# Performance work log

Measured on AMD Instinct MI355X. Metric: run time of the kernel, lower is better.

The kernel has to match this reference:

```python
import jax, jax.numpy as jnp
import numpy as np

B, T, C = 4, 1024, 1024
H, D = 16, 64


def setup_inputs() -> dict:
    key = jax.random.key(0)
    ks = jax.random.split(key, 5)
    sc = 0.02
    x = jax.random.normal(ks[0], (B, T, C), dtype=jnp.float32)
    Wq = jax.random.normal(ks[1], (H, C, D), dtype=jnp.float32) * sc
    Wk = jax.random.normal(ks[2], (H, C, D), dtype=jnp.float32) * sc
    Wv = jax.random.normal(ks[3], (H, C, D), dtype=jnp.float32) * sc
    Wp = jax.random.normal(ks[4], (H * D, C), dtype=jnp.float32) * sc
    bp = jnp.zeros((C,), dtype=jnp.float32)
    return {"x": x, "Wq": Wq, "Wk": Wk, "Wv": Wv, "Wp": Wp, "bp": bp}


def reference(x, Wq, Wk, Wv, Wp, bp):
    # per-head projections (bias-free, as in nanoGPT Head)
    q = jnp.einsum('btc,hcd->bhtd', x, Wq)
    k = jnp.einsum('btc,hcd->bhtd', x, Wk)
    v = jnp.einsum('btc,hcd->bhtd', x, Wv)
    scale = 1.0 / jnp.sqrt(jnp.asarray(D, dtype=x.dtype))
    scores = jnp.einsum('bhtd,bhsd->bhts', q, k) * scale  # [B,H,T,T]
    causal = jnp.tril(jnp.ones((T, T), dtype=bool))
    scores = jnp.where(causal, scores, jnp.asarray(-jnp.inf, dtype=scores.dtype))
    attn = jax.nn.softmax(scores, axis=-1)
    out = jnp.einsum('bhts,bhsd->bhtd', attn, v)  # [B,H,T,D]
    out = out.transpose(0, 2, 1, 3).reshape(B, T, H * D)  # concat heads
    return out @ Wp + bp  # final projection (dropout=0)
```

## Files before the change

kernel.cpp:

```cpp
#include <hip/hip_runtime.h>
#include <hip/hip_bf16.h>

typedef unsigned short u16;
typedef __bf16 bf16x8 __attribute__((ext_vector_type(8)));
typedef float floatx4 __attribute__((ext_vector_type(4)));

#define SB 4
#define ST 1024
#define SC 1024
#define SH 16
#define SD 64

__device__ __forceinline__ u16 f2bf(float f) {
    unsigned int u = __builtin_bit_cast(unsigned int, f);
    u += 0x7fffu + ((u >> 16) & 1u);
    return (u16)(u >> 16);
}

__device__ __forceinline__ void gload16(const u16* g, u16* l) {
    __builtin_amdgcn_global_load_lds(
        (const __attribute__((address_space(1))) unsigned int*)g,
        (__attribute__((address_space(3))) unsigned int*)l, 16, 0, 0);
}

__global__ void k_prep(const float* __restrict__ x,
                       const float* __restrict__ Wq, const float* __restrict__ Wk,
                       const float* __restrict__ Wv, const float* __restrict__ Wp,
                       u16* __restrict__ xb, u16* __restrict__ Wqkv, u16* __restrict__ Wpt) {
    __shared__ float tile[64 * 65];
    const int id = blockIdx.x, tid = threadIdx.x;
    if (id < 4096) {
        int i = id * 256 + tid;
        float4 v = ((const float4*)x)[i];
        uint2 o;
        o.x = (unsigned)f2bf(v.x) | ((unsigned)f2bf(v.y) << 16);
        o.y = (unsigned)f2bf(v.z) | ((unsigned)f2bf(v.w) << 16);
        ((uint2*)xb)[i] = o;
    } else if (id < 4864) {
        const int id1 = id - 4096;
        const int qkv = id1 >> 8, rem = id1 & 255, h = rem >> 4, c0 = (rem & 15) * 64;
        const float* src = qkv == 0 ? Wq : (qkv == 1 ? Wk : Wv);
        #pragma unroll
        for (int i = 0; i < 16; ++i) {
            int idx = tid + i * 256;
            int r = idx >> 6, d = idx & 63;
            tile[r * 65 + d] = src[(h * SC + c0 + r) * SD + d];
        }
        __syncthreads();
        #pragma unroll
        for (int i = 0; i < 16; ++i) {
            int idx = tid + i * 256;
            int d = idx >> 6, cc = idx & 63;
            Wqkv[(qkv * 1024 + h * SD + d) * SC + c0 + cc] = f2bf(tile[cc * 65 + d]);
        }
    } else {
        const int id2 = id - 4864;
        const int n0 = (id2 & 15) * 64, k0 = (id2 >> 4) * 64;
        #pragma unroll
        for (int i = 0; i < 16; ++i) {
            int idx = tid + i * 256;
            int r = idx >> 6, nn = idx & 63;
            tile[r * 65 + nn] = Wp[(k0 + r) * SC + n0 + nn];
        }
        __syncthreads();
        #pragma unroll
        for (int i = 0; i < 16; ++i) {
            int idx = tid + i * 256;
            int nr = idx >> 6, kk = idx & 63;
            Wpt[(n0 + nr) * (SH * SD) + k0 + kk] = f2bf(tile[kk * 65 + nr]);
        }
    }
}

__launch_bounds__(256)
__global__ void k_gemm(const u16* __restrict__ A, const u16* __restrict__ Bt,
                       int M, int N, int K,
                       u16* __restrict__ Qb, u16* __restrict__ Kb, u16* __restrict__ Vt) {
    constexpr int BM = 128, BN = 64, SM = 4, SN = 2;
    __shared__ u16 Als[2][BM * 64];
    __shared__ u16 Bls[2][BN * 64];
    const int tid = threadIdx.x, lane = tid & 63, w = tid >> 6;
    const int quad = lane >> 4, l16 = lane & 15;
    const int sr = lane >> 3, sc = lane & 7;
    const int nt = N / BN;
    const int m0 = (blockIdx.x / nt) * BM, n0 = (blockIdx.x % nt) * BN;
    const int wm = (w >> 1) * 64, wn = (w & 1) * 32;

    auto stage = [&](int buf, int k0) {
        #pragma unroll
        for (int i = 0; i < 4; ++i) {
            int rb = (w * 4 + i) * 8;
            gload16(&A[(long)(m0 + rb + sr) * K + k0 + ((sc ^ sr) << 3)], &Als[buf][rb * 64]);
        }
        #pragma unroll
        for (int i = 0; i < 2; ++i) {
            int rb = (w * 2 + i) * 8;
            gload16(&Bt[(long)(n0 + rb + sr) * K + k0 + ((sc ^ sr) << 3)], &Bls[buf][rb * 64]);
        }
    };

    floatx4 acc[SM][SN] = {};
    const int niter = K / 64;
    stage(0, 0);
    for (int it = 0; it < niter; ++it) {
        const int buf = it & 1;
        __syncthreads();
        if (it + 1 < niter) stage(buf ^ 1, (it + 1) * 64);
        bf16x8 af[SM][2], bfr[SN][2];
        #pragma unroll
        for (int sm = 0; sm < SM; ++sm) {
            int row = wm + sm * 16 + l16;
            #pragma unroll
            for (int ks = 0; ks < 2; ++ks)
                af[sm][ks] = *(const bf16x8*)&Als[buf][row * 64 + (((ks * 4 + quad) ^ (row & 7)) << 3)];
        }
        #pragma unroll
        for (int sn = 0; sn < SN; ++sn) {
            int row = wn + sn * 16 + l16;
            #pragma unroll
            for (int ks = 0; ks < 2; ++ks)
                bfr[sn][ks] = *(const bf16x8*)&Bls[buf][row * 64 + (((ks * 4 + quad) ^ (row & 7)) << 3)];
        }
        #pragma unroll
        for (int ks = 0; ks < 2; ++ks)
            #pragma unroll
            for (int sm = 0; sm < SM; ++sm)
                #pragma unroll
                for (int sn = 0; sn < SN; ++sn)
                    acc[sm][sn] = __builtin_amdgcn_mfma_f32_16x16x32_bf16(bfr[sn][ks], af[sm][ks], acc[sm][sn], 0, 0, 0);
    }
    const int qkv = n0 >> 10, h = (n0 & 1023) >> 6;
    const float qs = qkv == 0 ? 0.18033688011112042f : 1.0f;
    #pragma unroll
    for (int sm = 0; sm < SM; ++sm) {
        const int m = m0 + wm + sm * 16 + l16;
        const int bb = m >> 10, t = m & 1023;
        #pragma unroll
        for (int sn = 0; sn < SN; ++sn) {
            const int d0 = wn + sn * 16 + (quad << 2);
            u16 pk[4];
            #pragma unroll
            for (int r = 0; r < 4; ++r) pk[r] = f2bf(acc[sm][sn][r] * qs);
            if (qkv == 2) {
                const long vb = (long)(bb * SH + h) * SD * ST + t;
                #pragma unroll
                for (int r = 0; r < 4; ++r) Vt[vb + (long)(d0 + r) * ST] = pk[r];
            } else {
                u16* dst = qkv == 0 ? Qb : Kb;
                *(uint2*)&dst[(((long)(bb * SH + h) * ST + t) << 6) + d0] = *(uint2*)pk;
            }
        }
    }
}

__launch_bounds__(256)
__global__ void k_oproj(const u16* __restrict__ A, const u16* __restrict__ Bt,
                        const float* __restrict__ bias, float* __restrict__ Cout) {
    constexpr int K = 1024, N = 1024;
    __shared__ u16 Als[4][64 * 64];
    __shared__ u16 Bls[4][64 * 64];
    const int tid = threadIdx.x, lane = tid & 63, w = tid >> 6;
    const int quad = lane >> 4, l16 = lane & 15;
    const int sr = lane >> 3, sc = lane & 7;
    const int m0 = (blockIdx.x >> 4) * 64, n0 = (blockIdx.x & 15) * 64;
    const int wm = (w >> 1) * 32, wn = (w & 1) * 32;

    floatx4 acc[2][2] = {};
    for (int kb = 0; kb < 4; ++kb) {
        const int k0 = kb * 256;
        #pragma unroll
        for (int seg = 0; seg < 4; ++seg) {
            #pragma unroll
            for (int i = 0; i < 2; ++i) {
                int rb = (w * 2 + i) * 8;
                gload16(&A[(long)(m0 + rb + sr) * K + k0 + seg * 64 + ((sc ^ sr) << 3)], &Als[seg][rb * 64]);
                gload16(&Bt[(long)(n0 + rb + sr) * K + k0 + seg * 64 + ((sc ^ sr) << 3)], &Bls[seg][rb * 64]);
            }
        }
        __syncthreads();
        #pragma unroll
        for (int seg = 0; seg < 4; ++seg) {
            bf16x8 af[2][2], bfr[2][2];
            #pragma unroll
            for (int sm = 0; sm < 2; ++sm) {
                int row = wm + sm * 16 + l16;
                #pragma unroll
                for (int ks = 0; ks < 2; ++ks)
                    af[sm][ks] = *(const bf16x8*)&Als[seg][row * 64 + (((ks * 4 + quad) ^ (row & 7)) << 3)];
            }
            #pragma unroll
            for (int sn = 0; sn < 2; ++sn) {
                int row = wn + sn * 16 + l16;
                #pragma unroll
                for (int ks = 0; ks < 2; ++ks)
                    bfr[sn][ks] = *(const bf16x8*)&Bls[seg][row * 64 + (((ks * 4 + quad) ^ (row & 7)) << 3)];
            }
            #pragma unroll
            for (int ks = 0; ks < 2; ++ks)
                #pragma unroll
                for (int sm = 0; sm < 2; ++sm)
                    #pragma unroll
                    for (int sn = 0; sn < 2; ++sn)
                        acc[sm][sn] = __builtin_amdgcn_mfma_f32_16x16x32_bf16(bfr[sn][ks], af[sm][ks], acc[sm][sn], 0, 0, 0);
        }
        if (kb < 3) __syncthreads();
    }
    #pragma unroll
    for (int sn = 0; sn < 2; ++sn) {
        const int nb = n0 + wn + sn * 16 + (quad << 2);
        const float4 bv = *(const float4*)&bias[nb];
        #pragma unroll
        for (int sm = 0; sm < 2; ++sm) {
            const int m = m0 + wm + sm * 16 + l16;
            float4 o;
            o.x = acc[sm][sn][0] + bv.x;
            o.y = acc[sm][sn][1] + bv.y;
            o.z = acc[sm][sn][2] + bv.z;
            o.w = acc[sm][sn][3] + bv.w;
            *(float4*)&Cout[(long)m * N + nb] = o;
        }
    }
}

__launch_bounds__(256)
__global__ void k_attn(const u16* __restrict__ Qg, const u16* __restrict__ Kg,
                       const u16* __restrict__ Vtg, u16* __restrict__ Og) {
    __shared__ u16 Kls[2][64 * 64];
    __shared__ u16 Vls[2][64 * 64];
    __shared__ u16 Pls[64 * 64];
    const int tid = threadIdx.x, lane = tid & 63, w = tid >> 6;
    const int quad = lane >> 4, l16 = lane & 15;
    const int sr = lane >> 3, sc = lane & 7;
    const int tile = 15 - (blockIdx.x >> 6);
    const int bh = blockIdx.x & 63;
    const int t0 = tile * 64;
    const int b = bh >> 4, h = bh & 15;
    const u16* Qbh = Qg + (long)bh * ST * SD;
    const u16* Kbh = Kg + (long)bh * ST * SD;
    const u16* Vbh = Vtg + (long)bh * SD * ST;

    bf16x8 qf[2];
    {
        const u16* qrow = Qbh + (t0 + w * 16 + l16) * SD;
        qf[0] = *(const bf16x8*)&qrow[quad * 8];
        qf[1] = *(const bf16x8*)&qrow[32 + quad * 8];
    }
    floatx4 oacc[4] = {};
    float lsum = 0.f;
    const int myt = t0 + w * 16 + l16;
    const int rowP = w * 16 + l16;

    auto stage = [&](int buf, int s0) {
        #pragma unroll
        for (int i = 0; i < 2; ++i) {
            int rb = (w * 2 + i) * 8;
            gload16(&Kbh[(s0 + rb + sr) * SD + ((sc ^ sr) << 3)], &Kls[buf][rb * 64]);
            gload16(&Vbh[(rb + sr) * ST + s0 + ((sc ^ sr) << 3)], &Vls[buf][rb * 64]);
        }
    };

    stage(0, 0);
    for (int j = 0; j <= tile; ++j) {
        const int buf = j & 1;
        const int s0 = j * 64;
        __syncthreads();
        if (j < tile) stage(buf ^ 1, s0 + 64);

        floatx4 sa[4] = {};
        #pragma unroll
        for (int sn = 0; sn < 4; ++sn) {
            int row = sn * 16 + l16;
            #pragma unroll
            for (int ks = 0; ks < 2; ++ks) {
                bf16x8 kf = *(const bf16x8*)&Kls[buf][row * 64 + (((ks * 4 + quad) ^ (row & 7)) << 3)];
                sa[sn] = __builtin_amdgcn_mfma_f32_16x16x32_bf16(kf, qf[ks], sa[sn], 0, 0, 0);
            }
        }
        const bool diag = (j == tile);
        #pragma unroll
        for (int sn = 0; sn < 4; ++sn) {
            const int sl = sn * 16 + (quad << 2);
            u16 pk[4];
            #pragma unroll
            for (int r = 0; r < 4; ++r) {
                float e = __builtin_exp2f(sa[sn][r]);
                if (diag && s0 + sl + r > myt) e = 0.f;
                lsum += e;
                pk[r] = (u16)(__builtin_bit_cast(unsigned int, e) >> 16);
            }
            *(uint2*)&Pls[rowP * 64 + (((sl >> 3) ^ (rowP & 7)) << 3) + ((quad & 1) << 2)] = *(uint2*)pk;
        }
        bf16x8 pf[2];
        #pragma unroll
        for (int ks = 0; ks < 2; ++ks)
            pf[ks] = *(const bf16x8*)&Pls[rowP * 64 + (((ks * 4 + quad) ^ (rowP & 7)) << 3)];
        #pragma unroll
        for (int dn = 0; dn < 4; ++dn) {
            int row = dn * 16 + l16;
            #pragma unroll
            for (int ks = 0; ks < 2; ++ks) {
                bf16x8 vf = *(const bf16x8*)&Vls[buf][row * 64 + (((ks * 4 + quad) ^ (row & 7)) << 3)];
                oacc[dn] = __builtin_amdgcn_mfma_f32_16x16x32_bf16(vf, pf[ks], oacc[dn], 0, 0, 0);
            }
        }
    }
    float l = lsum;
    l += __shfl_xor(l, 16);
    l += __shfl_xor(l, 32);
    const float inv = 1.0f / l;
    const long obase = ((long)(b * ST + myt) << 10) + h * SD;
    #pragma unroll
    for (int dn = 0; dn < 4; ++dn) {
        u16 pk[4];
        #pragma unroll
        for (int r = 0; r < 4; ++r) pk[r] = f2bf(oacc[dn][r] * inv);
        *(uint2*)&Og[obase + dn * 16 + (quad << 2)] = *(uint2*)pk;
    }
}

extern "C" void kernel_launch(void* const* d_in, const int* in_sizes, int n_in,
                              void* d_out, int out_size, void* d_ws, size_t ws_size,
                              hipStream_t stream) {
    const float* x  = (const float*)d_in[0];
    const float* Wq = (const float*)d_in[1];
    const float* Wk = (const float*)d_in[2];
    const float* Wv = (const float*)d_in[3];
    const float* Wp = (const float*)d_in[4];
    const float* bp = (const float*)d_in[5];
    float* out = (float*)d_out;

    char* ws = (char*)d_ws;
    u16* xb   = (u16*)(ws);
    u16* Wqkv = (u16*)(ws + (8ll  << 20));
    u16* Wpt  = (u16*)(ws + (14ll << 20));
    u16* Qb   = (u16*)(ws + (16ll << 20));
    u16* Kb   = (u16*)(ws + (24ll << 20));
    u16* Vt   = (u16*)(ws + (32ll << 20));
    u16* Ob   = (u16*)(ws + (40ll << 20));

    k_prep<<<5120, 256, 0, stream>>>(x, Wq, Wk, Wv, Wp, xb, Wqkv, Wpt);
    k_gemm<<<32 * 48, 256, 0, stream>>>(xb, Wqkv, 4096, 3072, 1024, Qb, Kb, Vt);
    k_attn<<<1024, 256, 0, stream>>>(Qb, Kb, Vt, Ob);
    k_oproj<<<1024, 256, 0, stream>>>(Ob, Wpt, bp, out);
}
```

Baseline: 161.1 us.

## Process 128 query rows per attention block to reuse K/V tiles

The attention kernel now handles a 128-row query tile per block, with each wave owning two 16-row subtiles. Every K/V tile staged in LDS therefore feeds twice as many MFMAs, halving global K/V traffic and the grid size to 512 blocks. The trade-off is more registers per thread (doubled accumulators and score tiles), a larger P buffer in LDS, coarser causal work imbalance, and fewer blocks to fill the CUs. The last two key tiles are masked on the diagonal.

```diff
diff --git a/kernel.cpp b/kernel.cpp
--- a/kernel.cpp
+++ b/kernel.cpp
@@ -227,28 +227,30 @@
                        const u16* __restrict__ Vtg, u16* __restrict__ Og) {
     __shared__ u16 Kls[2][64 * 64];
     __shared__ u16 Vls[2][64 * 64];
-    __shared__ u16 Pls[64 * 64];
+    __shared__ u16 Pls[128 * 64];
     const int tid = threadIdx.x, lane = tid & 63, w = tid >> 6;
     const int quad = lane >> 4, l16 = lane & 15;
     const int sr = lane >> 3, sc = lane & 7;
-    const int tile = 15 - (blockIdx.x >> 6);
+    const int qt = 7 - (blockIdx.x >> 6);
     const int bh = blockIdx.x & 63;
-    const int t0 = tile * 64;
+    const int t0 = qt * 128;
     const int b = bh >> 4, h = bh & 15;
     const u16* Qbh = Qg + (long)bh * ST * SD;
     const u16* Kbh = Kg + (long)bh * ST * SD;
     const u16* Vbh = Vtg + (long)bh * SD * ST;
 
-    bf16x8 qf[2];
-    {
-        const u16* qrow = Qbh + (t0 + w * 16 + l16) * SD;
-        qf[0] = *(const bf16x8*)&qrow[quad * 8];
-        qf[1] = *(const bf16x8*)&qrow[32 + quad * 8];
-    }
-    floatx4 oacc[4] = {};
-    float lsum = 0.f;
-    const int myt = t0 + w * 16 + l16;
-    const int rowP = w * 16 + l16;
+    bf16x8 qf[2][2];
+    int myt[2], rowP[2];
+    #pragma unroll
+    for (int mi = 0; mi < 2; ++mi) {
+        rowP[mi] = w * 32 + mi * 16 + l16;
+        myt[mi] = t0 + rowP[mi];
+        const u16* qrow = Qbh + (long)myt[mi] * SD;
+        qf[mi][0] = *(const bf16x8*)&qrow[quad * 8];
+        qf[mi][1] = *(const bf16x8*)&qrow[32 + quad * 8];
+    }
+    floatx4 oacc[2][4] = {};
+    float lsum[2] = {};
 
     auto stage = [&](int buf, int s0) {
         #pragma unroll
@@ -259,62 +261,73 @@
         }
     };
 
+    const int jn = 2 * qt + 2;
     stage(0, 0);
-    for (int j = 0; j <= tile; ++j) {
+    for (int j = 0; j < jn; ++j) {
         const int buf = j & 1;
         const int s0 = j * 64;
         __syncthreads();
-        if (j < tile) stage(buf ^ 1, s0 + 64);
-
-        floatx4 sa[4] = {};
+        if (j + 1 < jn) stage(buf ^ 1, s0 + 64);
+
+        floatx4 sa[2][4] = {};
         #pragma unroll
         for (int sn = 0; sn < 4; ++sn) {
             int row = sn * 16 + l16;
             #pragma unroll
             for (int ks = 0; ks < 2; ++ks) {
                 bf16x8 kf = *(const bf16x8*)&Kls[buf][row * 64 + (((ks * 4 + quad) ^ (row & 7)) << 3)];
-                sa[sn] = __builtin_amdgcn_mfma_f32_16x16x32_bf16(kf, qf[ks], sa[sn], 0, 0, 0);
-            }
-        }
-        const bool diag = (j == tile);
-        #pragma unroll
-        for (int sn = 0; sn < 4; ++sn) {
-            const int sl = sn * 16 + (quad << 2);
-            u16 pk[4];
-            #pragma unroll
-            for (int r = 0; r < 4; ++r) {
-                float e = __builtin_exp2f(sa[sn][r]);
-                if (diag && s0 + sl + r > myt) e = 0.f;
-                lsum += e;
-                pk[r] = (u16)(__builtin_bit_cast(unsigned int, e) >> 16);
-            }
-            *(uint2*)&Pls[rowP * 64 + (((sl >> 3) ^ (rowP & 7)) << 3) + ((quad & 1) << 2)] = *(uint2*)pk;
-        }
-        bf16x8 pf[2];
-        #pragma unroll
-        for (int ks = 0; ks < 2; ++ks)
-            pf[ks] = *(const bf16x8*)&Pls[rowP * 64 + (((ks * 4 + quad) ^ (rowP & 7)) << 3)];
+                sa[0][sn] = __builtin_amdgcn_mfma_f32_16x16x32_bf16(kf, qf[0][ks], sa[0][sn], 0, 0, 0);
+                sa[1][sn] = __builtin_amdgcn_mfma_f32_16x16x32_bf16(kf, qf[1][ks], sa[1][sn], 0, 0, 0);
+            }
+        }
+        const bool diag = (j >= jn - 2);
+        #pragma unroll
+        for (int mi = 0; mi < 2; ++mi) {
+            #pragma unroll
+            for (int sn = 0; sn < 4; ++sn) {
+                const int sl = sn * 16 + (quad << 2);
+                u16 pk[4];
+                #pragma unroll
+                for (int r = 0; r < 4; ++r) {
+                    float e = __builtin_exp2f(sa[mi][sn][r]);
+                    if (diag && s0 + sl + r > myt[mi]) e = 0.f;
+                    lsum[mi] += e;
+                    pk[r] = (u16)(__builtin_bit_cast(unsigned int, e) >> 16);
+                }
+                *(uint2*)&Pls[rowP[mi] * 64 + (((sl >> 3) ^ (rowP[mi] & 7)) << 3) + ((quad & 1) << 2)] = *(uint2*)pk;
+            }
+        }
+        bf16x8 pf[2][2];
+        #pragma unroll
+        for (int mi = 0; mi < 2; ++mi)
+            #pragma unroll
+            for (int ks = 0; ks < 2; ++ks)
+                pf[mi][ks] = *(const bf16x8*)&Pls[rowP[mi] * 64 + (((ks * 4 + quad) ^ (rowP[mi] & 7)) << 3)];
         #pragma unroll
         for (int dn = 0; dn < 4; ++dn) {
             int row = dn * 16 + l16;
             #pragma unroll
             for (int ks = 0; ks < 2; ++ks) {
                 bf16x8 vf = *(const bf16x8*)&Vls[buf][row * 64 + (((ks * 4 + quad) ^ (row & 7)) << 3)];
-                oacc[dn] = __builtin_amdgcn_mfma_f32_16x16x32_bf16(vf, pf[ks], oacc[dn], 0, 0, 0);
-            }
-        }
-    }
-    float l = lsum;
-    l += __shfl_xor(l, 16);
-    l += __shfl_xor(l, 32);
-    const float inv = 1.0f / l;
-    const long obase = ((long)(b * ST + myt) << 10) + h * SD;
+                oacc[0][dn] = __builtin_amdgcn_mfma_f32_16x16x32_bf16(vf, pf[0][ks], oacc[0][dn], 0, 0, 0);
+                oacc[1][dn] = __builtin_amdgcn_mfma_f32_16x16x32_bf16(vf, pf[1][ks], oacc[1][dn], 0, 0, 0);
+            }
+        }
+    }
     #pragma unroll
-    for (int dn = 0; dn < 4; ++dn) {
-        u16 pk[4];
-        #pragma unroll
-        for (int r = 0; r < 4; ++r) pk[r] = f2bf(oacc[dn][r] * inv);
-        *(uint2*)&Og[obase + dn * 16 + (quad << 2)] = *(uint2*)pk;
+    for (int mi = 0; mi < 2; ++mi) {
+        float l = lsum[mi];
+        l += __shfl_xor(l, 16);
+        l += __shfl_xor(l, 32);
+        const float inv = 1.0f / l;
+        const long obase = ((long)(b * ST + myt[mi]) << 10) + h * SD;
+        #pragma unroll
+        for (int dn = 0; dn < 4; ++dn) {
+            u16 pk[4];
+            #pragma unroll
+            for (int r = 0; r < 4; ++r) pk[r] = f2bf(oacc[mi][dn][r] * inv);
+            *(uint2*)&Og[obase + dn * 16 + (quad << 2)] = *(uint2*)pk;
+        }
     }
 }
 
@@ -340,6 +353,6 @@
 
     k_prep<<<5120, 256, 0, stream>>>(x, Wq, Wk, Wv, Wp, xb, Wqkv, Wpt);
     k_gemm<<<32 * 48, 256, 0, stream>>>(xb, Wqkv, 4096, 3072, 1024, Qb, Kb, Vt);
-    k_attn<<<1024, 256, 0, stream>>>(Qb, Kb, Vt, Ob);
+    k_attn<<<512, 256, 0, stream>>>(Qb, Kb, Vt, Ob);
     k_oproj<<<1024, 256, 0, stream>>>(Ob, Wpt, bp, out);
 }
```

New measurement: 171.8 us. 6.7% more time.

## Shrink QKV GEMM K-tile to 32 and double-buffer output projection

Applied to the files above, without the earlier changes.

The QKV projection GEMM now stages 32-wide K slices instead of 64, which halves its LDS footprint and doubles the number of loop iterations and barriers. Its swizzle is changed to a 4-way XOR to match. The output projection drops its load-all-then-compute scheme over 256-wide chunks in favour of a 64-wide double-buffered pipeline that overlaps global-to-LDS loads with MFMA. This cuts LDS use so more blocks can be resident, at the cost of more synchronisation per unit of work.

```diff
diff --git a/kernel.cpp b/kernel.cpp
--- a/kernel.cpp
+++ b/kernel.cpp
@@ -77,57 +77,50 @@
                        int M, int N, int K,
                        u16* __restrict__ Qb, u16* __restrict__ Kb, u16* __restrict__ Vt) {
     constexpr int BM = 128, BN = 64, SM = 4, SN = 2;
-    __shared__ u16 Als[2][BM * 64];
-    __shared__ u16 Bls[2][BN * 64];
+    __shared__ u16 Als[2][BM * 32];
+    __shared__ u16 Bls[2][BN * 32];
     const int tid = threadIdx.x, lane = tid & 63, w = tid >> 6;
     const int quad = lane >> 4, l16 = lane & 15;
-    const int sr = lane >> 3, sc = lane & 7;
+    const int sr = lane >> 2, sc = lane & 3;
     const int nt = N / BN;
     const int m0 = (blockIdx.x / nt) * BM, n0 = (blockIdx.x % nt) * BN;
     const int wm = (w >> 1) * 64, wn = (w & 1) * 32;
 
     auto stage = [&](int buf, int k0) {
         #pragma unroll
-        for (int i = 0; i < 4; ++i) {
-            int rb = (w * 4 + i) * 8;
-            gload16(&A[(long)(m0 + rb + sr) * K + k0 + ((sc ^ sr) << 3)], &Als[buf][rb * 64]);
-        }
-        #pragma unroll
         for (int i = 0; i < 2; ++i) {
-            int rb = (w * 2 + i) * 8;
-            gload16(&Bt[(long)(n0 + rb + sr) * K + k0 + ((sc ^ sr) << 3)], &Bls[buf][rb * 64]);
+            int rb = (w * 2 + i) * 16;
+            gload16(&A[(long)(m0 + rb + sr) * K + k0 + ((sc ^ (sr & 3)) << 3)], &Als[buf][rb * 32]);
+        }
+        {
+            int rb = w * 16;
+            gload16(&Bt[(long)(n0 + rb + sr) * K + k0 + ((sc ^ (sr & 3)) << 3)], &Bls[buf][rb * 32]);
         }
     };
 
     floatx4 acc[SM][SN] = {};
-    const int niter = K / 64;
+    const int niter = K / 32;
     stage(0, 0);
     for (int it = 0; it < niter; ++it) {
         const int buf = it & 1;
         __syncthreads();
-        if (it + 1 < niter) stage(buf ^ 1, (it + 1) * 64);
-        bf16x8 af[SM][2], bfr[SN][2];
+        if (it + 1 < niter) stage(buf ^ 1, (it + 1) * 32);
+        bf16x8 af[SM], bfr[SN];
         #pragma unroll
         for (int sm = 0; sm < SM; ++sm) {
             int row = wm + sm * 16 + l16;
-            #pragma unroll
-            for (int ks = 0; ks < 2; ++ks)
-                af[sm][ks] = *(const bf16x8*)&Als[buf][row * 64 + (((ks * 4 + quad) ^ (row & 7)) << 3)];
+            af[sm] = *(const bf16x8*)&Als[buf][row * 32 + ((quad ^ (row & 3)) << 3)];
         }
         #pragma unroll
         for (int sn = 0; sn < SN; ++sn) {
             int row = wn + sn * 16 + l16;
-            #pragma unroll
-            for (int ks = 0; ks < 2; ++ks)
-                bfr[sn][ks] = *(const bf16x8*)&Bls[buf][row * 64 + (((ks * 4 + quad) ^ (row & 7)) << 3)];
-        }
-        #pragma unroll
-        for (int ks = 0; ks < 2; ++ks)
-            #pragma unroll
-            for (int sm = 0; sm < SM; ++sm)
-                #pragma unroll
-                for (int sn = 0; sn < SN; ++sn)
-                    acc[sm][sn] = __builtin_amdgcn_mfma_f32_16x16x32_bf16(bfr[sn][ks], af[sm][ks], acc[sm][sn], 0, 0, 0);
+            bfr[sn] = *(const bf16x8*)&Bls[buf][row * 32 + ((quad ^ (row & 3)) << 3)];
+        }
+        #pragma unroll
+        for (int sm = 0; sm < SM; ++sm)
+            #pragma unroll
+            for (int sn = 0; sn < SN; ++sn)
+                acc[sm][sn] = __builtin_amdgcn_mfma_f32_16x16x32_bf16(bfr[sn], af[sm], acc[sm][sn], 0, 0, 0);
     }
     const int qkv = n0 >> 10, h = (n0 & 1023) >> 6;
     const float qs = qkv == 0 ? 0.18033688011112042f : 1.0f;
@@ -157,53 +150,51 @@
 __global__ void k_oproj(const u16* __restrict__ A, const u16* __restrict__ Bt,
                         const float* __restrict__ bias, float* __restrict__ Cout) {
     constexpr int K = 1024, N = 1024;
-    __shared__ u16 Als[4][64 * 64];
-    __shared__ u16 Bls[4][64 * 64];
+    __shared__ u16 Als[2][64 * 64];
+    __shared__ u16 Bls[2][64 * 64];
     const int tid = threadIdx.x, lane = tid & 63, w = tid >> 6;
     const int quad = lane >> 4, l16 = lane & 15;
     const int sr = lane >> 3, sc = lane & 7;
     const int m0 = (blockIdx.x >> 4) * 64, n0 = (blockIdx.x & 15) * 64;
     const int wm = (w >> 1) * 32, wn = (w & 1) * 32;
 
+    auto stage = [&](int buf, int k0) {
+        #pragma unroll
+        for (int i = 0; i < 2; ++i) {
+            int rb = (w * 2 + i) * 8;
+            gload16(&A[(long)(m0 + rb + sr) * K + k0 + ((sc ^ sr) << 3)], &Als[buf][rb * 64]);
+            gload16(&Bt[(long)(n0 + rb + sr) * K + k0 + ((sc ^ sr) << 3)], &Bls[buf][rb * 64]);
+        }
+    };
+
     floatx4 acc[2][2] = {};
-    for (int kb = 0; kb < 4; ++kb) {
-        const int k0 = kb * 256;
-        #pragma unroll
-        for (int seg = 0; seg < 4; ++seg) {
-            #pragma unroll
-            for (int i = 0; i < 2; ++i) {
-                int rb = (w * 2 + i) * 8;
-                gload16(&A[(long)(m0 + rb + sr) * K + k0 + seg * 64 + ((sc ^ sr) << 3)], &Als[seg][rb * 64]);
-                gload16(&Bt[(long)(n0 + rb + sr) * K + k0 + seg * 64 + ((sc ^ sr) << 3)], &Bls[seg][rb * 64]);
-            }
-        }
-        __syncthreads();
-        #pragma unroll
-        for (int seg = 0; seg < 4; ++seg) {
-            bf16x8 af[2][2], bfr[2][2];
-            #pragma unroll
-            for (int sm = 0; sm < 2; ++sm) {
-                int row = wm + sm * 16 + l16;
+    stage(0, 0);
+    for (int it = 0; it < 16; ++it) {
+        const int buf = it & 1;
+        __syncthreads();
+        if (it + 1 < 16) stage(buf ^ 1, (it + 1) * 64);
+        bf16x8 af[2][2], bfr[2][2];
+        #pragma unroll
+        for (int sm = 0; sm < 2; ++sm) {
+            int row = wm + sm * 16 + l16;
+            #pragma unroll
+            for (int ks = 0; ks < 2; ++ks)
+                af[sm][ks] = *(const bf16x8*)&Als[buf][row * 64 + (((ks * 4 + quad) ^ (row & 7)) << 3)];
+        }
+        #pragma unroll
+        for (int sn = 0; sn < 2; ++sn) {
+            int row = wn + sn * 16 + l16;
+            #pragma unroll
+            for (int ks = 0; ks < 2; ++ks)
+                bfr[sn][ks] = *(const bf16x8*)&Bls[buf][row * 64 + (((ks * 4 + quad) ^ (row & 7)) << 3)];
+        }
+        #pragma unroll
+        for (int ks = 0; ks < 2; ++ks)
+            #pragma unroll
+            for (int sm = 0; sm < 2; ++sm)
                 #pragma unroll
-                for (int ks = 0; ks < 2; ++ks)
-                    af[sm][ks] = *(const bf16x8*)&Als[seg][row * 64 + (((ks * 4 + quad) ^ (row & 7)) << 3)];
-            }
-            #pragma unroll
-            for (int sn = 0; sn < 2; ++sn) {
-                int row = wn + sn * 16 + l16;
-                #pragma unroll
-                for (int ks = 0; ks < 2; ++ks)
-                    bfr[sn][ks] = *(const bf16x8*)&Bls[seg][row * 64 + (((ks * 4 + quad) ^ (row & 7)) << 3)];
-            }
-            #pragma unroll
-            for (int ks = 0; ks < 2; ++ks)
-                #pragma unroll
-                for (int sm = 0; sm < 2; ++sm)
-                    #pragma unroll
-                    for (int sn = 0; sn < 2; ++sn)
-                        acc[sm][sn] = __builtin_amdgcn_mfma_f32_16x16x32_bf16(bfr[sn][ks], af[sm][ks], acc[sm][sn], 0, 0, 0);
-        }
-        if (kb < 3) __syncthreads();
+                for (int sn = 0; sn < 2; ++sn)
+                    acc[sm][sn] = __builtin_amdgcn_mfma_f32_16x16x32_bf16(bfr[sn][ks], af[sm][ks], acc[sm][sn], 0, 0, 0);
     }
     #pragma unroll
     for (int sn = 0; sn < 2; ++sn) {
```

After: 176.3 us. 1.09x slower.
